# Kernel tuning notes

Measured on AMD Instinct MI355X. Metric: run time of the kernel, lower is better.

Reference implementation:

```python
import jax, jax.numpy as jnp
import numpy as np

PH, PW = 7, 7          # output_size
GRID = 2               # sampling_ratio
SCALES = (0.25, 0.125, 0.0625, 0.03125)  # 2^round(log2(feat/img)) per level
LVL_MIN, LVL_MAX = 2, 5                  # -log2(scales[0]), -log2(scales[-1])
CANON_SCALE, CANON_LVL = 224.0, 4.0
EPS = 1e-6


def setup_inputs() -> dict:
    key = jax.random.key(0)
    ks = jax.random.split(key, 6)
    B, C = 2, 256
    sizes = [(200, 200), (100, 100), (50, 50), (25, 25)]
    inp = {f"feat{i}": jax.random.normal(ks[i], (B, C, h, w), jnp.float32)
           for i, (h, w) in enumerate(sizes)}
    Nb = 256
    # boxes in 800x800 image coords, x1y1 + positive wh so 0<=x1<x2, 0<=y1<y2
    xy = jax.random.uniform(ks[4], (B, Nb, 2), jnp.float32, 0.0, 700.0)
    wh = jax.random.uniform(ks[5], (B, Nb, 2), jnp.float32, 32.0, 512.0)
    inp["boxes"] = jnp.concatenate([xy, xy + wh], axis=-1)
    return inp


def _roi_align_level(feat, b_idx, rois, scale):
    """torchvision roi_align, aligned=False. feat [B,C,H,W], rois [R,4] -> [R,C,PH,PW]."""
    H, W = feat.shape[2], feat.shape[3]
    x1 = rois[:, 0] * scale
    y1 = rois[:, 1] * scale
    x2 = rois[:, 2] * scale
    y2 = rois[:, 3] * scale
    roi_w = jnp.maximum(x2 - x1, 1.0)
    roi_h = jnp.maximum(y2 - y1, 1.0)
    bin_w = roi_w / PW
    bin_h = roi_h / PH
    # sub-bin sampling offsets: (bin + (i+0.5)/grid) for each bin, flattened [PH*GRID]
    gy = (jnp.arange(PH, dtype=jnp.float32)[:, None]
          + (jnp.arange(GRID, dtype=jnp.float32)[None, :] + 0.5) / GRID).reshape(-1)
    gx = (jnp.arange(PW, dtype=jnp.float32)[:, None]
          + (jnp.arange(GRID, dtype=jnp.float32)[None, :] + 0.5) / GRID).reshape(-1)
    ys = y1[:, None] + gy[None, :] * bin_h[:, None]   # [R, PH*G]
    xs = x1[:, None] + gx[None, :] * bin_w[:, None]   # [R, PW*G]
    y = ys[:, :, None]                                 # [R, PH*G, 1]
    x = xs[:, None, :]                                 # [R, 1, PW*G]
    valid = (y >= -1.0) & (y <= H) & (x >= -1.0) & (x <= W)
    yc = jnp.clip(y, 0.0, H - 1)
    xc = jnp.clip(x, 0.0, W - 1)
    yl = jnp.floor(yc).astype(jnp.int32)
    xl = jnp.floor(xc).astype(jnp.int32)
    yh = jnp.minimum(yl + 1, H - 1)
    xh = jnp.minimum(xl + 1, W - 1)
    ly = yc - yl.astype(yc.dtype)
    lx = xc - xl.astype(xc.dtype)
    hy = 1.0 - ly
    hx = 1.0 - lx
    b = b_idx[:, None, None]

    def gather(yi, xi):
        # advanced indexing with slice in channel dim -> [R, PH*G, PW*G, C]
        return feat[b, :, yi, xi]

    val = ((hy * hx)[..., None] * gather(yl, xl)
           + (hy * lx)[..., None] * gather(yl, xh)
           + (ly * hx)[..., None] * gather(yh, xl)
           + (ly * lx)[..., None] * gather(yh, xh))
    val = jnp.where(valid[..., None], val, 0.0)
    R, C = rois.shape[0], feat.shape[1]
    # average over the GRIDxGRID sampling points of each bin
    val = val.reshape(R, PH, GRID, PW, GRID, C).mean(axis=(2, 4))  # [R,PH,PW,C]
    return jnp.transpose(val, (0, 3, 1, 2))                        # [R,C,PH,PW]


def reference(feat0, feat1, feat2, feat3, boxes):
    feats = [feat0, feat1, feat2, feat3]
    B, Nb = boxes.shape[0], boxes.shape[1]
    rois = boxes.reshape(-1, 4)                               # convert_to_roi_format
    b_idx = jnp.repeat(jnp.arange(B), Nb)
    # LevelMapper (FPN eq. 1)
    s = jnp.sqrt(jnp.maximum((rois[:, 2] - rois[:, 0]) * (rois[:, 3] - rois[:, 1]), 0.0))
    lvl = jnp.floor(CANON_LVL + jnp.log2(s / CANON_SCALE + EPS))
    lvl = jnp.clip(lvl, LVL_MIN, LVL_MAX).astype(jnp.int32) - LVL_MIN  # [R] in [0,3]
    out = jnp.zeros((rois.shape[0], feats[0].shape[1], PH, PW), feats[0].dtype)
    for l, (f, sc) in enumerate(zip(feats, SCALES)):
        pooled = _roi_align_level(f, b_idx, rois, sc)
        out = jnp.where((lvl == l)[:, None, None, None], pooled, out)
    return out
```

## Files before the change

kernel.cpp:

```cpp
#include <hip/hip_runtime.h>


#define PHW 49
#define NCHUNK 8
#define CH 32
#define PSIZE 1024

#define BARRIER_KEEP_VMCNT()                                   \
    do {                                                       \
        asm volatile("s_waitcnt lgkmcnt(0)" ::: "memory");     \
        __builtin_amdgcn_s_barrier();                          \
    } while (0)

__global__ __launch_bounds__(256) void msroi_kernel(
    const float* __restrict__ f0, const float* __restrict__ f1,
    const float* __restrict__ f2, const float* __restrict__ f3,
    const float* __restrict__ boxes, float* __restrict__ out)
{
    const int C = 256, Nb = 256;
    const int r = blockIdx.x;
    const int chunk = blockIdx.y;
    const int tid = threadIdx.x;
    const int b = r / Nb;

    const int bin = tid >> 2;
    const int q   = tid & 3;
    const bool active = bin < PHW;

    const float x1b = boxes[r * 4 + 0];
    const float y1b = boxes[r * 4 + 1];
    const float x2b = boxes[r * 4 + 2];
    const float y2b = boxes[r * 4 + 3];
    const float area = fmaxf((x2b - x1b) * (y2b - y1b), 0.0f);
    const float s = sqrtf(area);
    float lv = floorf(4.0f + log2f(s / 224.0f + 1e-6f));
    lv = fminf(fmaxf(lv, 2.0f), 5.0f);
    const int lvl = (int)lv - 2;

    const float* feat;
    int H, W;
    float scale;
    switch (lvl) {
        case 0:  feat = f0; H = 200; W = 200; scale = 0.25f;    break;
        case 1:  feat = f1; H = 100; W = 100; scale = 0.125f;   break;
        case 2:  feat = f2; H = 50;  W = 50;  scale = 0.0625f;  break;
        default: feat = f3; H = 25;  W = 25;  scale = 0.03125f; break;
    }
    const int HW = H * W;

    const float x1 = x1b * scale, y1 = y1b * scale;
    const float x2 = x2b * scale, y2 = y2b * scale;
    const float roi_w = fmaxf(x2 - x1, 1.0f);
    const float roi_h = fmaxf(y2 - y1, 1.0f);
    const float bin_w = roi_w * (1.0f / 7.0f);
    const float bin_h = roi_h * (1.0f / 7.0f);

    const float ys0 = fminf(fmaxf(y1 + 0.25f * bin_h, 0.0f), (float)(H - 1));
    const float ys1 = fminf(fmaxf(y1 + 6.75f * bin_h, 0.0f), (float)(H - 1));
    const float xs0 = fminf(fmaxf(x1 + 0.25f * bin_w, 0.0f), (float)(W - 1));
    const float xs1 = fminf(fmaxf(x1 + 6.75f * bin_w, 0.0f), (float)(W - 1));
    const int row0 = (int)floorf(ys0);
    const int row1 = min((int)floorf(ys1) + 1, H - 1);
    const int col0 = (int)floorf(xs0);
    const int col1 = min((int)floorf(xs1) + 1, W - 1);
    const int prows = row1 - row0 + 1;
    const int pcols = col1 - col0 + 1;
    const int psize = prows * pcols;
    const int wstride = W - pcols;
    const float inv_pcols = 1.0f / (float)pcols;

    int goff[4];
#pragma unroll
    for (int k = 0; k < 4; ++k) {
        const int e = tid + k * 256;
        const int ec = min(e, psize - 1);
        const int rr = (int)floorf(((float)ec + 0.5f) * inv_pcols);
        goff[k] = ec + rr * wstride;
    }
    const int kmax = (psize + 255) >> 8;

    int   offs[4];
    float wts[4];
    {
        const int bb = active ? bin : 0;
        const int ph = bb / 7;
        const int pw = bb - ph * 7;
        const int iy = q >> 1, ix = q & 1;
        const float gy = (float)ph + ((float)iy + 0.5f) * 0.5f;
        const float gx = (float)pw + ((float)ix + 0.5f) * 0.5f;
        const float y = y1 + gy * bin_h;
        const float x = x1 + gx * bin_w;
        const bool valid = (y >= -1.0f) && (y <= (float)H) &&
                           (x >= -1.0f) && (x <= (float)W);
        const float yc = fminf(fmaxf(y, 0.0f), (float)(H - 1));
        const float xc = fminf(fmaxf(x, 0.0f), (float)(W - 1));
        const int yl = (int)floorf(yc);
        const int xl = (int)floorf(xc);
        const int yh = min(yl + 1, H - 1);
        const int xh = min(xl + 1, W - 1);
        const float ly = yc - (float)yl;
        const float lx = xc - (float)xl;
        const float hy = 1.0f - ly, hx = 1.0f - lx;
        const float m = valid ? 0.25f : 0.0f;
        const int ry0 = (yl - row0) * pcols, ry1 = (yh - row0) * pcols;
        const int cx0 = xl - col0, cx1 = xh - col0;
        offs[0] = ry0 + cx0;  wts[0] = hy * hx * m;
        offs[1] = ry0 + cx1;  wts[1] = hy * lx * m;
        offs[2] = ry1 + cx0;  wts[2] = ly * hx * m;
        offs[3] = ry1 + cx1;  wts[3] = ly * lx * m;
    }

    __shared__ float4 lds4[PSIZE];

    const int cbase = chunk * CH;
    const float* __restrict__ fch =
        feat + (size_t)(b * C + cbase) * HW + (row0 * W + col0);
    float* __restrict__ outp =
        out + (size_t)r * C * PHW + (size_t)cbase * PHW;

    float4 bufA[4], bufB[4];

#define LOADR(BUF, CCV)                                                    \
    do {                                                                   \
        const float* __restrict__ g0 = fch + (size_t)((CCV) + 0) * HW;     \
        const float* __restrict__ g1 = fch + (size_t)((CCV) + 1) * HW;     \
        const float* __restrict__ g2 = fch + (size_t)((CCV) + 2) * HW;     \
        const float* __restrict__ g3 = fch + (size_t)((CCV) + 3) * HW;     \
        _Pragma("unroll")                                                  \
        for (int k = 0; k < 4; ++k) {                                      \
            if (k < kmax) {       \
                BUF[k].x = g0[goff[k]];                                    \
                BUF[k].y = g1[goff[k]];                                    \
                BUF[k].z = g2[goff[k]];                                    \
                BUF[k].w = g3[goff[k]];                                    \
            }                                                              \
        }                                                                  \
    } while (0)

#define WRITELDS(BUF)                                                      \
    do {                                                                   \
        _Pragma("unroll")                                                  \
        for (int k = 0; k < 4; ++k)                                        \
            if (k < kmax) lds4[tid + k * 256] = BUF[k];                    \
    } while (0)

#define COMPUTE(CCV)                                                       \
    do {                                                                   \
        if (active) {                                                      \
            float4 a = make_float4(0.0f, 0.0f, 0.0f, 0.0f);                \
            _Pragma("unroll")                                              \
            for (int j = 0; j < 4; ++j) {                                  \
                const float4 v = lds4[offs[j]];                            \
                a.x += wts[j] * v.x;                                       \
                a.y += wts[j] * v.y;                                       \
                a.z += wts[j] * v.z;                                       \
                a.w += wts[j] * v.w;                                       \
            }                                                              \
            a.x += __shfl_xor(a.x, 1); a.y += __shfl_xor(a.y, 1);          \
            a.z += __shfl_xor(a.z, 1); a.w += __shfl_xor(a.w, 1);          \
            a.x += __shfl_xor(a.x, 2); a.y += __shfl_xor(a.y, 2);          \
            a.z += __shfl_xor(a.z, 2); a.w += __shfl_xor(a.w, 2);          \
            const float vout = (q == 0) ? a.x : (q == 1) ? a.y             \
                             : (q == 2) ? a.z : a.w;                       \
            outp[(size_t)((CCV) + q) * PHW + bin] = vout;                  \
        }                                                                  \
    } while (0)

    LOADR(bufA, 0);
    LOADR(bufB, 4);

#pragma unroll
    for (int c = 0; c < CH; c += 8) {
        BARRIER_KEEP_VMCNT();
        WRITELDS(bufA);
        if (c + 8 < CH) LOADR(bufA, c + 8);
        BARRIER_KEEP_VMCNT();
        COMPUTE(c);

        BARRIER_KEEP_VMCNT();
        WRITELDS(bufB);
        if (c + 12 < CH) LOADR(bufB, c + 12);
        BARRIER_KEEP_VMCNT();
        COMPUTE(c + 4);
    }
#undef LOADR
#undef WRITELDS
#undef COMPUTE
}

extern "C" void kernel_launch(void* const* d_in, const int* in_sizes, int n_in,
                              void* d_out, int out_size, void* d_ws, size_t ws_size,
                              hipStream_t stream) {
    const float* f0 = (const float*)d_in[0];
    const float* f1 = (const float*)d_in[1];
    const float* f2 = (const float*)d_in[2];
    const float* f3 = (const float*)d_in[3];
    const float* boxes = (const float*)d_in[4];
    float* out = (float*)d_out;

    const int R = in_sizes[4] / 4;
    dim3 grid(R, NCHUNK);
    msroi_kernel<<<grid, 256, 0, stream>>>(f0, f1, f2, f3, boxes, out);
}
```

Baseline: 183.4 us.

## Double-buffer LDS patch tile to halve barriers and drop kmax guards

Turns the single shared-memory patch tile into two ping-pong slices, so compute on one slice overlaps the write of the next and each 4-channel step needs one barrier instead of two. It also removes the kmax guard, so every thread always issues all four global loads and LDS writes; clamped offsets keep these in bounds but add redundant traffic for small patches. Launch bounds now request a minimum of 5 blocks per unit, which may limit registers, while LDS use doubles to 32KB per block, which can cap occupancy.

Result: no change. 180.1 us (-1.8%).

```diff
diff --git a/kernel.cpp b/kernel.cpp
--- a/kernel.cpp
+++ b/kernel.cpp
@@ -12,7 +12,7 @@
         __builtin_amdgcn_s_barrier();                          \
     } while (0)
 
-__global__ __launch_bounds__(256) void msroi_kernel(
+__global__ __launch_bounds__(256, 5) void msroi_kernel(
     const float* __restrict__ f0, const float* __restrict__ f1,
     const float* __restrict__ f2, const float* __restrict__ f3,
     const float* __restrict__ boxes, float* __restrict__ out)
@@ -77,7 +77,6 @@
         const int rr = (int)floorf(((float)ec + 0.5f) * inv_pcols);
         goff[k] = ec + rr * wstride;
     }
-    const int kmax = (psize + 255) >> 8;
 
     int   offs[4];
     float wts[4];
@@ -110,7 +109,7 @@
         offs[3] = ry1 + cx1;  wts[3] = ly * lx * m;
     }
 
-    __shared__ float4 lds4[PSIZE];
+    __shared__ float4 lds4[2][PSIZE];
 
     const int cbase = chunk * CH;
     const float* __restrict__ fch =
@@ -128,29 +127,27 @@
         const float* __restrict__ g3 = fch + (size_t)((CCV) + 3) * HW;     \
         _Pragma("unroll")                                                  \
         for (int k = 0; k < 4; ++k) {                                      \
-            if (k < kmax) {       \
-                BUF[k].x = g0[goff[k]];                                    \
-                BUF[k].y = g1[goff[k]];                                    \
-                BUF[k].z = g2[goff[k]];                                    \
-                BUF[k].w = g3[goff[k]];                                    \
-            }                                                              \
+            BUF[k].x = g0[goff[k]];                                        \
+            BUF[k].y = g1[goff[k]];                                        \
+            BUF[k].z = g2[goff[k]];                                        \
+            BUF[k].w = g3[goff[k]];                                        \
         }                                                                  \
     } while (0)
 
-#define WRITELDS(BUF)                                                      \
+#define WRITELDS(SL, BUF)                                                  \
     do {                                                                   \
         _Pragma("unroll")                                                  \
         for (int k = 0; k < 4; ++k)                                        \
-            if (k < kmax) lds4[tid + k * 256] = BUF[k];                    \
-    } while (0)
-
-#define COMPUTE(CCV)                                                       \
+            lds4[SL][tid + k * 256] = BUF[k];                              \
+    } while (0)
+
+#define COMPUTE(SL, CCV)                                                   \
     do {                                                                   \
         if (active) {                                                      \
             float4 a = make_float4(0.0f, 0.0f, 0.0f, 0.0f);                \
             _Pragma("unroll")                                              \
             for (int j = 0; j < 4; ++j) {                                  \
-                const float4 v = lds4[offs[j]];                            \
+                const float4 v = lds4[SL][offs[j]];                        \
                 a.x += wts[j] * v.x;                                       \
                 a.y += wts[j] * v.y;                                       \
                 a.z += wts[j] * v.z;                                       \
@@ -168,20 +165,24 @@
 
     LOADR(bufA, 0);
     LOADR(bufB, 4);
+    WRITELDS(0, bufA);
+    LOADR(bufA, 8);
+    BARRIER_KEEP_VMCNT();
 
 #pragma unroll
-    for (int c = 0; c < CH; c += 8) {
+    for (int i = 0; i < 8; ++i) {
+        const int cur = i & 1, nxt = cur ^ 1;
+        COMPUTE(cur, i * 4);
+        if (i < 7) {
+            if (i & 1) {
+                WRITELDS(nxt, bufA);
+                if (i + 3 < 8) LOADR(bufA, (i + 3) * 4);
+            } else {
+                WRITELDS(nxt, bufB);
+                if (i + 3 < 8) LOADR(bufB, (i + 3) * 4);
+            }
+        }
         BARRIER_KEEP_VMCNT();
-        WRITELDS(bufA);
-        if (c + 8 < CH) LOADR(bufA, c + 8);
-        BARRIER_KEEP_VMCNT();
-        COMPUTE(c);
-
-        BARRIER_KEEP_VMCNT();
-        WRITELDS(bufB);
-        if (c + 12 < CH) LOADR(bufB, c + 12);
-        BARRIER_KEEP_VMCNT();
-        COMPUTE(c + 4);
     }
 #undef LOADR
 #undef WRITELDS
```
